# Optimization experiments

Hardware: AMD Instinct MI355X
Metric: run time of the kernel (lower is better)

## Reference

```python
import jax, jax.numpy as jnp
import numpy as np

B, S, D = 4, 4096, 1024  # S = maxlength * 2, D = hidden_dim * 2 (bi-rnn)
MAXLENGTH = 2048
NEG_BIG = -2.0 ** 31


def setup_inputs() -> dict:
    key = jax.random.key(0)
    k1, k2, k3, k4, k5 = jax.random.split(key, 5)
    inputs = jax.random.normal(k1, (B, S, D), dtype=jnp.float32)
    length = jax.random.randint(k2, (B,), 1, MAXLENGTH + 1, dtype=jnp.int32)
    # torch code requires max(length)*2 == maxlength*2 for expand() to work
    length = length.at[0].set(MAXLENGTH)
    scale = 1.0 / np.sqrt(D)
    Wq = jax.random.normal(k3, (D, D), dtype=jnp.float32) * scale
    Wk = jax.random.normal(k4, (D, D), dtype=jnp.float32) * scale
    Wv = jax.random.normal(k5, (D, D), dtype=jnp.float32) * scale
    return {"inputs": inputs, "length": length, "Wq": Wq, "Wk": Wk,
            "Wv": Wv, "maxlength": MAXLENGTH}


def reference(inputs, length, Wq, Wk, Wv, maxlength):
    # nn.Linear (bias=False): y = x @ W.T
    Q = inputs @ Wq.T                      # [B, S, D]
    K = inputs @ Wk.T                      # [B, S, D]
    V = inputs @ Wv.T                      # [B, S, D]
    max_len = maxlength * 2
    sent_len = length.astype(jnp.float32) * 2.0      # [B]
    # key-padding mask, broadcast over query dim: [B, 1, max_len]
    mask = (jnp.arange(max_len, dtype=jnp.float32)[None, :] < sent_len[:, None])[:, None, :]
    alpha = jnp.einsum('bqd,bkd->bqk', Q, K)         # [B, S, S] (no 1/sqrt(d) scaling, as in source)
    alpha = jnp.where(mask, alpha, NEG_BIG)
    alpha = jax.nn.softmax(alpha, axis=2)
    out = jnp.einsum('bqk,bkd->bqd', alpha, V)       # [B, S, D]
    return out
```

## Files before the change

### kernel.cpp

```cpp
#include <hip/hip_runtime.h>


typedef __attribute__((ext_vector_type(4))) float floatx4;
typedef __attribute__((ext_vector_type(4))) int intx4;
typedef __attribute__((ext_vector_type(8))) short shortx8;
typedef unsigned short ushort_t;

__device__ __forceinline__ ushort_t f2bf(float f) {
  union { float f; unsigned u; } x; x.f = f;
  unsigned r = x.u + 0x7fffu + ((x.u >> 16) & 1u);
  return (ushort_t)(r >> 16);
}
__device__ __forceinline__ float bf2f(ushort_t h) {
  union { unsigned u; float f; } x; x.u = ((unsigned)h) << 16; return x.f;
}
__device__ __forceinline__ void quant8(float v, char& qh, char& ql) {
  float vs = v * 16.0f;
  float h = rintf(vs);
  h = fminf(fmaxf(h, -127.f), 127.f);
  float l = rintf((vs - h) * 256.0f);
  l = fminf(fmaxf(l, -127.f), 127.f);
  qh = (char)(int)h; ql = (char)(int)l;
}
__device__ __forceinline__ void quant8w(float v, char& qh, char& ql) {
  float vs = v * 512.0f;
  float h = rintf(vs);
  h = fminf(fmaxf(h, -127.f), 127.f);
  float l = rintf((vs - h) * 256.0f);
  l = fminf(fmaxf(l, -127.f), 127.f);
  qh = (char)(int)h; ql = (char)(int)l;
}

__device__ __forceinline__ void gload_lds16(const void* g, void* l) {
  __builtin_amdgcn_global_load_lds(
      (__attribute__((address_space(1))) void*)(uintptr_t)g,
      (__attribute__((address_space(3))) void*)(unsigned)(uintptr_t)l,
      16, 0, 0);
}

template<int TM, int TN, int NA, int NB, int OMODE, int LMODE>
__global__ __launch_bounds__(256)
void gemm_bt(const ushort_t* __restrict__ A0g, const ushort_t* __restrict__ A1g,
             const ushort_t* __restrict__ B0g, const ushort_t* __restrict__ B1g,
             void* __restrict__ C0v, void* __restrict__ C1v,
             int K, int lda, int ldc, long bstride,
             const int* __restrict__ lenp, int b0, long sA, long sB, long sC)
{
  constexpr int BM = TM * 32, BN = TN * 32;
  constexpr int LA = TM / 2, LB = TN / 2;
  constexpr bool DUAL = (NA == 2) && (NB == 2);
  __shared__ ushort_t As[NA][BM][32];
  __shared__ ushort_t Bs[NB][BN][32];

  const int tid = threadIdx.x;
  const int z = blockIdx.z;
  const long row0 = (long)blockIdx.x * BM;
  const long col0 = (long)blockIdx.y * BN;

  int kend = K;
  if constexpr (LMODE == 2) {
    const int sent = lenp[b0 + z] * 2;
    kend = (sent + 127) & ~127;
  } else if constexpr (LMODE == 3) {
    const int sent = lenp[row0 >> 12] * 2;
    if ((int)(row0 & 4095) >= ((sent + 127) & ~127)) return;
  }

  const int sr = tid >> 2, scol = (tid & 3) * 8;
  const ushort_t* pA0 = A0g + z * sA + (row0 + sr) * (long)lda + scol;
  const ushort_t* pA1 = (NA == 2) ? A1g + z * sA + (row0 + sr) * (long)lda + scol : nullptr;
  const ushort_t* pB0 = B0g + z * sB + (col0 + sr) * (long)K + scol;
  const ushort_t* pB1 = (NB == 2) ? B1g + z * sB + (col0 + sr) * (long)K + scol : nullptr;
  ushort_t* lA0 = &As[0][sr][scol];
  ushort_t* lA1 = (NA == 2) ? &As[NA - 1][sr][scol] : nullptr;
  ushort_t* lB0 = &Bs[0][sr][scol];
  ushort_t* lB1 = (NB == 2) ? &Bs[NB - 1][sr][scol] : nullptr;
  const long jA = 64 * (long)lda, jB = 64 * (long)K;

  const int wid = tid >> 6, lane = tid & 63;
  const int wm = (wid >> 1) * (BM / 2), wn = (wid & 1) * (BN / 2);
  const int lr = lane & 15, lq = lane >> 4;

  floatx4 acc[TM][TN] = {};

  for (int k0 = 0; k0 < kend; k0 += 32) {
#pragma unroll
    for (int j = 0; j < LA; ++j) {
      gload_lds16(pA0 + k0 + j * jA, lA0 + j * 2048);
      if constexpr (NA == 2) gload_lds16(pA1 + k0 + j * jA, lA1 + j * 2048);
    }
#pragma unroll
    for (int j = 0; j < LB; ++j) {
      gload_lds16(pB0 + k0 + j * jB, lB0 + j * 2048);
      if constexpr (NB == 2) gload_lds16(pB1 + k0 + j * jB, lB1 + j * 2048);
    }
    __syncthreads();

    shortx8 ah[TM], al[TM], bh[TN], bl[TN];
#pragma unroll
    for (int t = 0; t < TM; ++t) {
      ah[t] = *(const shortx8*)&As[0][wm + t * 16 + lr][lq * 8];
      if constexpr (NA == 2) al[t] = *(const shortx8*)&As[1][wm + t * 16 + lr][lq * 8];
    }
#pragma unroll
    for (int t = 0; t < TN; ++t) {
      bh[t] = *(const shortx8*)&Bs[0][wn + t * 16 + lr][lq * 8];
      if constexpr (NB == 2) bl[t] = *(const shortx8*)&Bs[1][wn + t * 16 + lr][lq * 8];
    }
#pragma unroll
    for (int mt = 0; mt < TM; ++mt)
#pragma unroll
      for (int nt = 0; nt < TN; ++nt) {
        acc[mt][nt] = __builtin_amdgcn_mfma_f32_16x16x32_bf16(ah[mt], bh[nt], acc[mt][nt], 0, 0, 0);
        if constexpr (DUAL) {
          acc[mt][nt] = __builtin_amdgcn_mfma_f32_16x16x32_bf16(ah[mt], bl[nt], acc[mt][nt], 0, 0, 0);
          acc[mt][nt] = __builtin_amdgcn_mfma_f32_16x16x32_bf16(al[mt], bh[nt], acc[mt][nt], 0, 0, 0);
        }
      }
    __syncthreads();
  }

#pragma unroll
  for (int mt = 0; mt < TM; ++mt) {
#pragma unroll
    for (int nt = 0; nt < TN; ++nt) {
      long col = col0 + wn + nt * 16 + lr;
      if constexpr (OMODE == 2) {
        long row = row0 + wm + mt * 16 + lq * 4;
        long bb = row >> 12, s = row & 4095;
        ushort4 pk;
        pk.x = f2bf(acc[mt][nt][0]); pk.y = f2bf(acc[mt][nt][1]);
        pk.z = f2bf(acc[mt][nt][2]); pk.w = f2bf(acc[mt][nt][3]);
        *(ushort4*)&((ushort_t*)C0v)[bb * bstride + col * ldc + s] = pk;
      } else {
#pragma unroll
        for (int r = 0; r < 4; ++r) {
          long row = row0 + wm + mt * 16 + lq * 4 + r;
          float v = acc[mt][nt][r];
          if constexpr (OMODE == 0) {
            ((float*)C0v)[z * sC + row * ldc + col] = v;
          } else {
            char qh, ql;
            quant8(v, qh, ql);
            ((char*)C0v)[row * ldc + col] = qh;
            ((char*)C1v)[row * ldc + col] = ql;
          }
        }
      }
    }
  }
}

template<int LMODE>
__global__ __launch_bounds__(256)
void proj_i8(const char* __restrict__ Ah, const char* __restrict__ Al,
             const char* __restrict__ Bh, const char* __restrict__ Bl,
             char* __restrict__ Ch, char* __restrict__ Cl,
             const int* __restrict__ lenp)
{
  __shared__ char As[2][128][64];
  __shared__ char Bs[2][64][64];
  const int tid = threadIdx.x;
  const long row0 = (long)blockIdx.x * 128;
  const long col0 = (long)blockIdx.y * 64;
  if constexpr (LMODE == 3) {
    const int sent = lenp[row0 >> 12] * 2;
    if ((int)(row0 & 4095) >= ((sent + 127) & ~127)) return;
  }

  const int sr = tid >> 2, sc16 = (tid & 3) * 16;
  const char* pA0 = Ah + (row0 + sr) * 1024 + sc16;
  const char* pA1 = Al + (row0 + sr) * 1024 + sc16;
  const char* pB0 = Bh + (col0 + sr) * 1024 + sc16;
  const char* pB1 = Bl + (col0 + sr) * 1024 + sc16;
  char* lA0 = &As[0][sr][sc16];
  char* lA1 = &As[1][sr][sc16];
  char* lB0 = &Bs[0][sr][sc16];
  char* lB1 = &Bs[1][sr][sc16];

  const int wid = tid >> 6, lane = tid & 63;
  const int wm = (wid >> 1) * 64, wn = (wid & 1) * 32;
  const int lr = lane & 15, lq = lane >> 4;

  intx4 acc1[4][2] = {};
  intx4 acc2[4][2] = {};
  intx4 acc3[4][2] = {};

  for (int k0 = 0; k0 < 1024; k0 += 64) {
#pragma unroll
    for (int j = 0; j < 2; ++j) {
      gload_lds16(pA0 + k0 + j * 65536, lA0 + j * 4096);
      gload_lds16(pA1 + k0 + j * 65536, lA1 + j * 4096);
    }
    gload_lds16(pB0 + k0, lB0);
    gload_lds16(pB1 + k0, lB1);
    __syncthreads();

    intx4 ah[4], al[4], bh[2], bl[2];
#pragma unroll
    for (int t = 0; t < 4; ++t) {
      ah[t] = *(const intx4*)&As[0][wm + t * 16 + lr][lq * 16];
      al[t] = *(const intx4*)&As[1][wm + t * 16 + lr][lq * 16];
    }
#pragma unroll
    for (int t = 0; t < 2; ++t) {
      bh[t] = *(const intx4*)&Bs[0][wn + t * 16 + lr][lq * 16];
      bl[t] = *(const intx4*)&Bs[1][wn + t * 16 + lr][lq * 16];
    }
#pragma unroll
    for (int mt = 0; mt < 4; ++mt)
#pragma unroll
      for (int nt = 0; nt < 2; ++nt) {
        acc1[mt][nt] = __builtin_amdgcn_mfma_i32_16x16x64_i8(ah[mt], bh[nt], acc1[mt][nt], 0, 0, 0);
        acc2[mt][nt] = __builtin_amdgcn_mfma_i32_16x16x64_i8(ah[mt], bl[nt], acc2[mt][nt], 0, 0, 0);
        acc2[mt][nt] = __builtin_amdgcn_mfma_i32_16x16x64_i8(al[mt], bh[nt], acc2[mt][nt], 0, 0, 0);
        acc3[mt][nt] = __builtin_amdgcn_mfma_i32_16x16x64_i8(al[mt], bl[nt], acc3[mt][nt], 0, 0, 0);
      }
    __syncthreads();
  }

#pragma unroll
  for (int mt = 0; mt < 4; ++mt)
#pragma unroll
    for (int nt = 0; nt < 2; ++nt) {
      long col = col0 + wn + nt * 16 + lr;
#pragma unroll
      for (int r = 0; r < 4; ++r) {
        long row = row0 + wm + mt * 16 + lq * 4 + r;
        float v = ((float)acc1[mt][nt][r]
                   + (float)acc2[mt][nt][r] * (1.0f / 256.0f)
                   + (float)acc3[mt][nt][r] * (1.0f / 65536.0f)) * (1.0f / 8192.0f);
        char qh, ql;
        quant8(v, qh, ql);
        Ch[row * 1024 + col] = qh;
        Cl[row * 1024 + col] = ql;
      }
    }
}

__global__ __launch_bounds__(256)
void qk_i8(const char* __restrict__ Qh, const char* __restrict__ Ql,
           const char* __restrict__ Kh, const char* __restrict__ Kl,
           short* __restrict__ sc, const int* __restrict__ lenp, int b)
{
  __shared__ char As[2][128][64];
  __shared__ char Bs[2][64][64];
  const int tid = threadIdx.x;
  const long row0 = (long)blockIdx.x * 128;
  const long col0 = (long)blockIdx.y * 64;
  const int sent = lenp[b] * 2;
  if (col0 >= sent) return;

  const int sr = tid >> 2, sc16 = (tid & 3) * 16;
  const char* pA0 = Qh + (row0 + sr) * 1024 + sc16;
  const char* pA1 = Ql + (row0 + sr) * 1024 + sc16;
  const char* pB0 = Kh + (col0 + sr) * 1024 + sc16;
  const char* pB1 = Kl + (col0 + sr) * 1024 + sc16;
  char* lA0 = &As[0][sr][sc16];
  char* lA1 = &As[1][sr][sc16];
  char* lB0 = &Bs[0][sr][sc16];
  char* lB1 = &Bs[1][sr][sc16];

  const int wid = tid >> 6, lane = tid & 63;
  const int wm = (wid >> 1) * 64, wn = (wid & 1) * 32;
  const int lr = lane & 15, lq = lane >> 4;

  intx4 acc1[4][2] = {};
  intx4 acc2[4][2] = {};

  for (int k0 = 0; k0 < 1024; k0 += 64) {
#pragma unroll
    for (int j = 0; j < 2; ++j) {
      gload_lds16(pA0 + k0 + j * 65536, lA0 + j * 4096);
      gload_lds16(pA1 + k0 + j * 65536, lA1 + j * 4096);
    }
    gload_lds16(pB0 + k0, lB0);
    gload_lds16(pB1 + k0, lB1);
    __syncthreads();

    intx4 ah[4], al[4], bh[2], bl[2];
#pragma unroll
    for (int t = 0; t < 4; ++t) {
      ah[t] = *(const intx4*)&As[0][wm + t * 16 + lr][lq * 16];
      al[t] = *(const intx4*)&As[1][wm + t * 16 + lr][lq * 16];
    }
#pragma unroll
    for (int t = 0; t < 2; ++t) {
      bh[t] = *(const intx4*)&Bs[0][wn + t * 16 + lr][lq * 16];
      bl[t] = *(const intx4*)&Bs[1][wn + t * 16 + lr][lq * 16];
    }
#pragma unroll
    for (int mt = 0; mt < 4; ++mt)
#pragma unroll
      for (int nt = 0; nt < 2; ++nt) {
        acc1[mt][nt] = __builtin_amdgcn_mfma_i32_16x16x64_i8(ah[mt], bh[nt], acc1[mt][nt], 0, 0, 0);
        acc2[mt][nt] = __builtin_amdgcn_mfma_i32_16x16x64_i8(ah[mt], bl[nt], acc2[mt][nt], 0, 0, 0);
        acc2[mt][nt] = __builtin_amdgcn_mfma_i32_16x16x64_i8(al[mt], bh[nt], acc2[mt][nt], 0, 0, 0);
      }
    __syncthreads();
  }

#pragma unroll
  for (int mt = 0; mt < 4; ++mt)
#pragma unroll
    for (int nt = 0; nt < 2; ++nt) {
      long col = col0 + wn + nt * 16 + lr;
#pragma unroll
      for (int r = 0; r < 4; ++r) {
        long row = row0 + wm + mt * 16 + lq * 4 + r;
        float v = (float)acc1[mt][nt][r] * 0.125f
                + (float)acc2[mt][nt][r] * (1.0f / 2048.0f);
        v = fminf(fmaxf(v, -32000.0f), 32000.0f);
        sc[row * 4096 + col] = (short)(int)rintf(v);
      }
    }
}

__global__ __launch_bounds__(256)
void cast_split(const float* __restrict__ in, ushort_t* __restrict__ hi,
                char* __restrict__ qh, char* __restrict__ ql, int n4) {
  int i = blockIdx.x * 256 + threadIdx.x;
  if (i < n4) {
    float4 v = ((const float4*)in)[i];
    ushort4 h;
    h.x = f2bf(v.x); h.y = f2bf(v.y); h.z = f2bf(v.z); h.w = f2bf(v.w);
    ((ushort4*)hi)[i] = h;
    char ax, bx, ay, by, az, bz, aw, bw;
    quant8(v.x, ax, bx); quant8(v.y, ay, by);
    quant8(v.z, az, bz); quant8(v.w, aw, bw);
    char4 a, b;
    a.x = ax; a.y = ay; a.z = az; a.w = aw;
    b.x = bx; b.y = by; b.z = bz; b.w = bw;
    ((char4*)qh)[i] = a;
    ((char4*)ql)[i] = b;
  }
}

__global__ __launch_bounds__(256)
void cast_wqk(const float* __restrict__ w0, const float* __restrict__ w1,
              char* __restrict__ h0, char* __restrict__ l0,
              char* __restrict__ h1, char* __restrict__ l1, int n4) {
  int i = blockIdx.x * 256 + threadIdx.x;
  if (i >= n4) return;
  const float* in = blockIdx.y ? w1 : w0;
  char* hp = blockIdx.y ? h1 : h0;
  char* lp = blockIdx.y ? l1 : l0;
  float4 v = ((const float4*)in)[i];
  char ax, bx, ay, by, az, bz, aw, bw;
  quant8w(v.x, ax, bx); quant8w(v.y, ay, by);
  quant8w(v.z, az, bz); quant8w(v.w, aw, bw);
  char4 a, b;
  a.x = ax; a.y = ay; a.z = az; a.w = aw;
  b.x = bx; b.y = by; b.z = bz; b.w = bw;
  ((char4*)hp)[i] = a;
  ((char4*)lp)[i] = b;
}

__global__ __launch_bounds__(256)
void cast_wv(const float* __restrict__ w, ushort_t* __restrict__ h, int n4) {
  int i = blockIdx.x * 256 + threadIdx.x;
  if (i >= n4) return;
  float4 v = ((const float4*)w)[i];
  ushort4 p;
  p.x = f2bf(v.x); p.y = f2bf(v.y); p.z = f2bf(v.z); p.w = f2bf(v.w);
  ((ushort4*)h)[i] = p;
}

__global__ __launch_bounds__(256)
void softmax_rows(short* __restrict__ scores, const int* __restrict__ length, int b0) {
  const long row = blockIdx.x;
  const int b = b0 + (int)(row >> 12);
  short* p = scores + row * 4096;
  const int sent = length[b] * 2;
  const int sentceil = (sent + 127) & ~127;
  const int tid = threadIdx.x;
  float vals[16];
  float mx = -3.4e38f;
  int nj = 0;
  for (int c = tid; c < sentceil; c += 256) {
    float v = (float)p[c] * (1.0f / 32.0f);
    v = (c < sent) ? v : -2147483648.0f;
    vals[nj++] = v;
    mx = fmaxf(mx, v);
  }
#pragma unroll
  for (int off = 32; off > 0; off >>= 1) mx = fmaxf(mx, __shfl_down(mx, off));
  __shared__ float red[8];
  if ((tid & 63) == 0) red[tid >> 6] = mx;
  __syncthreads();
  mx = fmaxf(fmaxf(red[0], red[1]), fmaxf(red[2], red[3]));
  float sum = 0.f;
  for (int j = 0; j < nj; ++j) { vals[j] = __expf(vals[j] - mx); sum += vals[j]; }
#pragma unroll
  for (int off = 32; off > 0; off >>= 1) sum += __shfl_down(sum, off);
  __syncthreads();
  if ((tid & 63) == 0) red[tid >> 6] = sum;
  __syncthreads();
  float inv = 1.0f / (red[0] + red[1] + red[2] + red[3]);
  ushort_t* pb = (ushort_t*)p;
  int j = 0;
  for (int c = tid; c < sentceil; c += 256) pb[c] = f2bf(vals[j++] * inv);
}

extern "C" void kernel_launch(void* const* d_in, const int* in_sizes, int n_in,
                              void* d_out, int out_size, void* d_ws, size_t ws_size,
                              hipStream_t stream) {
  const float* X   = (const float*)d_in[0];
  const int*   len = (const int*)d_in[1];
  const float* Wq  = (const float*)d_in[2];
  const float* Wk  = (const float*)d_in[3];
  const float* Wv  = (const float*)d_in[4];
  float* out = (float*)d_out;

  const int Bn = 4, S = 4096, D = 1024;
  const long MS = (long)Bn * S;

  char* w = (char*)d_ws;
  ushort_t* Xhi = (ushort_t*)w; w += MS * D * 2;
  char* Xh8 = w; w += MS * D;
  char* Xl8 = w; w += MS * D;
  char* Qh8 = w; w += MS * D;
  char* Ql8 = w; w += MS * D;
  char* Kh8 = w; w += MS * D;
  char* Kl8 = w; w += MS * D;
  ushort_t* Vt  = (ushort_t*)w; w += MS * D * 2;
  char* Wqh8 = w; w += (long)D * D;
  char* Wql8 = w; w += (long)D * D;
  char* Wkh8 = w; w += (long)D * D;
  char* Wkl8 = w; w += (long)D * D;
  ushort_t* Wvh = (ushort_t*)w; w += (long)D * D * 2;
  short* sc = (short*)d_ws;

  const int n4x = (int)(MS * D / 4);
  const int n4w = D * D / 4;
  cast_split<<<(n4x + 255) / 256, 256, 0, stream>>>(X, Xhi, Xh8, Xl8, n4x);
  cast_wqk<<<dim3((n4w + 255) / 256, 2), 256, 0, stream>>>(
      Wq, Wk, Wqh8, Wql8, Wkh8, Wkl8, n4w);
  cast_wv<<<(n4w + 255) / 256, 256, 0, stream>>>(Wv, Wvh, n4w);

  dim3 blk(256);
  proj_i8<0><<<dim3(MS / 128, D / 64), blk, 0, stream>>>(
      Xh8, Xl8, Wqh8, Wql8, Qh8, Ql8, len);
  proj_i8<3><<<dim3(MS / 128, D / 64), blk, 0, stream>>>(
      Xh8, Xl8, Wkh8, Wkl8, Kh8, Kl8, len);
  gemm_bt<4, 4, 1, 1, 2, 3><<<dim3(MS / 128, D / 128, 1), blk, 0, stream>>>(
      Xhi, nullptr, Wvh, nullptr, Vt, nullptr, D, D, S, (long)D * S,
      len, 0, 0, 0, 0);

  for (int b = 0; b < Bn; ++b) {
    const long so = (long)b * S * D;
    qk_i8<<<dim3(S / 128, S / 64), blk, 0, stream>>>(
        Qh8 + so, Ql8 + so, Kh8 + so, Kl8 + so, sc, len, b);
    softmax_rows<<<S, 256, 0, stream>>>(sc, len, b);
    gemm_bt<4, 2, 1, 1, 0, 2><<<dim3(S / 128, D / 64, 1), blk, 0, stream>>>(
        (const ushort_t*)sc, nullptr, Vt + (long)b * D * S, nullptr,
        out + so, nullptr, S, S, D, 0, len, b, 0, 0, 0);
  }
}
```

Before: 717.7 us.

## Double-buffer LDS tiles with vmcnt-based prefetch in all GEMM kernels

Adds double-buffered shared-memory staging to gemm_bt, proj_i8 and qk_i8. The next K tile is issued with global_load_lds before computing on the current one, and the code waits with explicit s_waitcnt vmcnt counts plus raw barriers, so load latency overlaps MFMA work. It also strips the unused dual/quant modes from gemm_bt and widens the PV GEMM tile from 128x64 to 128x128. The doubled LDS footprint may lower occupancy, and the hand-counted vmcnt waits are fragile if the compiler reorders memory operations.

```diff
diff --git a/kernel.cpp b/kernel.cpp
--- a/kernel.cpp
+++ b/kernel.cpp
@@ -38,28 +38,38 @@
       16, 0, 0);
 }
 
-template<int TM, int TN, int NA, int NB, int OMODE, int LMODE>
-__global__ __launch_bounds__(256)
-void gemm_bt(const ushort_t* __restrict__ A0g, const ushort_t* __restrict__ A1g,
-             const ushort_t* __restrict__ B0g, const ushort_t* __restrict__ B1g,
-             void* __restrict__ C0v, void* __restrict__ C1v,
-             int K, int lda, int ldc, long bstride,
-             const int* __restrict__ lenp, int b0, long sA, long sB, long sC)
+template<int N> __device__ __forceinline__ void wait_vm() {
+  static_assert(N == 0 || N == 4 || N == 6, "unsupported vmcnt");
+  if constexpr (N == 0) asm volatile("s_waitcnt vmcnt(0)" ::: "memory");
+  else if constexpr (N == 4) asm volatile("s_waitcnt vmcnt(4)" ::: "memory");
+  else if constexpr (N == 6) asm volatile("s_waitcnt vmcnt(6)" ::: "memory");
+}
+__device__ __forceinline__ void barrier_fenced() {
+  asm volatile("" ::: "memory");
+  __builtin_amdgcn_s_barrier();
+  asm volatile("" ::: "memory");
+}
+
+template<int TM, int TN, int OMODE, int LMODE>
+__global__ __launch_bounds__(256)
+void gemm_bt(const ushort_t* __restrict__ A0g, const ushort_t* __restrict__ B0g,
+             void* __restrict__ C0v, int K, int lda, int ldc, long bstride,
+             const int* __restrict__ lenp, int b0)
 {
   constexpr int BM = TM * 32, BN = TN * 32;
   constexpr int LA = TM / 2, LB = TN / 2;
-  constexpr bool DUAL = (NA == 2) && (NB == 2);
-  __shared__ ushort_t As[NA][BM][32];
-  __shared__ ushort_t Bs[NB][BN][32];
+  constexpr int NL = LA + LB;
+  constexpr int BUFA = BM * 32, BUFB = BN * 32;
+  __shared__ ushort_t As[2][BM][32];
+  __shared__ ushort_t Bs[2][BN][32];
 
   const int tid = threadIdx.x;
-  const int z = blockIdx.z;
   const long row0 = (long)blockIdx.x * BM;
   const long col0 = (long)blockIdx.y * BN;
 
   int kend = K;
   if constexpr (LMODE == 2) {
-    const int sent = lenp[b0 + z] * 2;
+    const int sent = lenp[b0] * 2;
     kend = (sent + 127) & ~127;
   } else if constexpr (LMODE == 3) {
     const int sent = lenp[row0 >> 12] * 2;
@@ -67,14 +77,10 @@
   }
 
   const int sr = tid >> 2, scol = (tid & 3) * 8;
-  const ushort_t* pA0 = A0g + z * sA + (row0 + sr) * (long)lda + scol;
-  const ushort_t* pA1 = (NA == 2) ? A1g + z * sA + (row0 + sr) * (long)lda + scol : nullptr;
-  const ushort_t* pB0 = B0g + z * sB + (col0 + sr) * (long)K + scol;
-  const ushort_t* pB1 = (NB == 2) ? B1g + z * sB + (col0 + sr) * (long)K + scol : nullptr;
-  ushort_t* lA0 = &As[0][sr][scol];
-  ushort_t* lA1 = (NA == 2) ? &As[NA - 1][sr][scol] : nullptr;
-  ushort_t* lB0 = &Bs[0][sr][scol];
-  ushort_t* lB1 = (NB == 2) ? &Bs[NB - 1][sr][scol] : nullptr;
+  const ushort_t* pA = A0g + (row0 + sr) * (long)lda + scol;
+  const ushort_t* pB = B0g + (col0 + sr) * (long)K + scol;
+  ushort_t* lA = &As[0][sr][scol];
+  ushort_t* lB = &Bs[0][sr][scol];
   const long jA = 64 * (long)lda, jB = 64 * (long)K;
 
   const int wid = tid >> 6, lane = tid & 63;
@@ -83,41 +89,37 @@
 
   floatx4 acc[TM][TN] = {};
 
-  for (int k0 = 0; k0 < kend; k0 += 32) {
-#pragma unroll
-    for (int j = 0; j < LA; ++j) {
-      gload_lds16(pA0 + k0 + j * jA, lA0 + j * 2048);
-      if constexpr (NA == 2) gload_lds16(pA1 + k0 + j * jA, lA1 + j * 2048);
-    }
-#pragma unroll
-    for (int j = 0; j < LB; ++j) {
-      gload_lds16(pB0 + k0 + j * jB, lB0 + j * 2048);
-      if constexpr (NB == 2) gload_lds16(pB1 + k0 + j * jB, lB1 + j * 2048);
-    }
-    __syncthreads();
-
-    shortx8 ah[TM], al[TM], bh[TN], bl[TN];
-#pragma unroll
-    for (int t = 0; t < TM; ++t) {
-      ah[t] = *(const shortx8*)&As[0][wm + t * 16 + lr][lq * 8];
-      if constexpr (NA == 2) al[t] = *(const shortx8*)&As[1][wm + t * 16 + lr][lq * 8];
-    }
-#pragma unroll
-    for (int t = 0; t < TN; ++t) {
-      bh[t] = *(const shortx8*)&Bs[0][wn + t * 16 + lr][lq * 8];
-      if constexpr (NB == 2) bl[t] = *(const shortx8*)&Bs[1][wn + t * 16 + lr][lq * 8];
-    }
+  auto stage = [&](int buf, int k0) {
+#pragma unroll
+    for (int j = 0; j < LA; ++j)
+      gload_lds16(pA + k0 + j * jA, lA + buf * BUFA + j * 2048);
+#pragma unroll
+    for (int j = 0; j < LB; ++j)
+      gload_lds16(pB + k0 + j * jB, lB + buf * BUFB + j * 2048);
+  };
+
+  const int nk = kend >> 5;
+  stage(0, 0);
+  for (int t = 0; t < nk; ++t) {
+    const int cur = t & 1;
+    if (t + 1 < nk) { stage(cur ^ 1, (t + 1) << 5); wait_vm<NL>(); }
+    else           { wait_vm<0>(); }
+    barrier_fenced();
+
+    shortx8 af[TM], bf[TN];
+#pragma unroll
+    for (int tt = 0; tt < TM; ++tt)
+      af[tt] = *(const shortx8*)&As[cur][wm + tt * 16 + lr][lq * 8];
+#pragma unroll
+    for (int tt = 0; tt < TN; ++tt)
+      bf[tt] = *(const shortx8*)&Bs[cur][wn + tt * 16 + lr][lq * 8];
 #pragma unroll
     for (int mt = 0; mt < TM; ++mt)
 #pragma unroll
-      for (int nt = 0; nt < TN; ++nt) {
-        acc[mt][nt] = __builtin_amdgcn_mfma_f32_16x16x32_bf16(ah[mt], bh[nt], acc[mt][nt], 0, 0, 0);
-        if constexpr (DUAL) {
-          acc[mt][nt] = __builtin_amdgcn_mfma_f32_16x16x32_bf16(ah[mt], bl[nt], acc[mt][nt], 0, 0, 0);
-          acc[mt][nt] = __builtin_amdgcn_mfma_f32_16x16x32_bf16(al[mt], bh[nt], acc[mt][nt], 0, 0, 0);
-        }
-      }
-    __syncthreads();
+      for (int nt = 0; nt < TN; ++nt)
+        acc[mt][nt] = __builtin_amdgcn_mfma_f32_16x16x32_bf16(af[mt], bf[nt], acc[mt][nt], 0, 0, 0);
+
+    barrier_fenced();
   }
 
 #pragma unroll
@@ -136,15 +138,7 @@
 #pragma unroll
         for (int r = 0; r < 4; ++r) {
           long row = row0 + wm + mt * 16 + lq * 4 + r;
-          float v = acc[mt][nt][r];
-          if constexpr (OMODE == 0) {
-            ((float*)C0v)[z * sC + row * ldc + col] = v;
-          } else {
-            char qh, ql;
-            quant8(v, qh, ql);
-            ((char*)C0v)[row * ldc + col] = qh;
-            ((char*)C1v)[row * ldc + col] = ql;
-          }
+          ((float*)C0v)[row * ldc + col] = acc[mt][nt][r];
         }
       }
     }
@@ -158,8 +152,8 @@
              char* __restrict__ Ch, char* __restrict__ Cl,
              const int* __restrict__ lenp)
 {
-  __shared__ char As[2][128][64];
-  __shared__ char Bs[2][64][64];
+  __shared__ char As[2][2][128][64];
+  __shared__ char Bs[2][2][64][64];
   const int tid = threadIdx.x;
   const long row0 = (long)blockIdx.x * 128;
   const long col0 = (long)blockIdx.y * 64;
@@ -173,10 +167,10 @@
   const char* pA1 = Al + (row0 + sr) * 1024 + sc16;
   const char* pB0 = Bh + (col0 + sr) * 1024 + sc16;
   const char* pB1 = Bl + (col0 + sr) * 1024 + sc16;
-  char* lA0 = &As[0][sr][sc16];
-  char* lA1 = &As[1][sr][sc16];
-  char* lB0 = &Bs[0][sr][sc16];
-  char* lB1 = &Bs[1][sr][sc16];
+  char* lA0 = &As[0][0][sr][sc16];
+  char* lA1 = &As[0][1][sr][sc16];
+  char* lB0 = &Bs[0][0][sr][sc16];
+  char* lB1 = &Bs[0][1][sr][sc16];
 
   const int wid = tid >> 6, lane = tid & 63;
   const int wm = (wid >> 1) * 64, wn = (wid & 1) * 32;
@@ -186,26 +180,33 @@
   intx4 acc2[4][2] = {};
   intx4 acc3[4][2] = {};
 
-  for (int k0 = 0; k0 < 1024; k0 += 64) {
+  auto stage = [&](int buf, int k0) {
 #pragma unroll
     for (int j = 0; j < 2; ++j) {
-      gload_lds16(pA0 + k0 + j * 65536, lA0 + j * 4096);
-      gload_lds16(pA1 + k0 + j * 65536, lA1 + j * 4096);
-    }
-    gload_lds16(pB0 + k0, lB0);
-    gload_lds16(pB1 + k0, lB1);
-    __syncthreads();
+      gload_lds16(pA0 + k0 + j * 65536, lA0 + buf * 16384 + j * 4096);
+      gload_lds16(pA1 + k0 + j * 65536, lA1 + buf * 16384 + j * 4096);
+    }
+    gload_lds16(pB0 + k0, lB0 + buf * 8192);
+    gload_lds16(pB1 + k0, lB1 + buf * 8192);
+  };
+
+  stage(0, 0);
+  for (int t = 0; t < 16; ++t) {
+    const int cur = t & 1;
+    if (t + 1 < 16) { stage(cur ^ 1, (t + 1) << 6); wait_vm<6>(); }
+    else           { wait_vm<0>(); }
+    barrier_fenced();
 
     intx4 ah[4], al[4], bh[2], bl[2];
 #pragma unroll
-    for (int t = 0; t < 4; ++t) {
-      ah[t] = *(const intx4*)&As[0][wm + t * 16 + lr][lq * 16];
-      al[t] = *(const intx4*)&As[1][wm + t * 16 + lr][lq * 16];
-    }
-#pragma unroll
-    for (int t = 0; t < 2; ++t) {
-      bh[t] = *(const intx4*)&Bs[0][wn + t * 16 + lr][lq * 16];
-      bl[t] = *(const intx4*)&Bs[1][wn + t * 16 + lr][lq * 16];
+    for (int tt = 0; tt < 4; ++tt) {
+      ah[tt] = *(const intx4*)&As[cur][0][wm + tt * 16 + lr][lq * 16];
+      al[tt] = *(const intx4*)&As[cur][1][wm + tt * 16 + lr][lq * 16];
+    }
+#pragma unroll
+    for (int tt = 0; tt < 2; ++tt) {
+      bh[tt] = *(const intx4*)&Bs[cur][0][wn + tt * 16 + lr][lq * 16];
+      bl[tt] = *(const intx4*)&Bs[cur][1][wn + tt * 16 + lr][lq * 16];
     }
 #pragma unroll
     for (int mt = 0; mt < 4; ++mt)
@@ -216,7 +217,7 @@
         acc2[mt][nt] = __builtin_amdgcn_mfma_i32_16x16x64_i8(al[mt], bh[nt], acc2[mt][nt], 0, 0, 0);
         acc3[mt][nt] = __builtin_amdgcn_mfma_i32_16x16x64_i8(al[mt], bl[nt], acc3[mt][nt], 0, 0, 0);
       }
-    __syncthreads();
+    barrier_fenced();
   }
 
 #pragma unroll
@@ -243,8 +244,8 @@
            const char* __restrict__ Kh, const char* __restrict__ Kl,
            short* __restrict__ sc, const int* __restrict__ lenp, int b)
 {
-  __shared__ char As[2][128][64];
-  __shared__ char Bs[2][64][64];
+  __shared__ char As[2][2][128][64];
+  __shared__ char Bs[2][2][64][64];
   const int tid = threadIdx.x;
   const long row0 = (long)blockIdx.x * 128;
   const long col0 = (long)blockIdx.y * 64;
@@ -256,10 +257,10 @@
   const char* pA1 = Ql + (row0 + sr) * 1024 + sc16;
   const char* pB0 = Kh + (col0 + sr) * 1024 + sc16;
   const char* pB1 = Kl + (col0 + sr) * 1024 + sc16;
-  char* lA0 = &As[0][sr][sc16];
-  char* lA1 = &As[1][sr][sc16];
-  char* lB0 = &Bs[0][sr][sc16];
-  char* lB1 = &Bs[1][sr][sc16];
+  char* lA0 = &As[0][0][sr][sc16];
+  char* lA1 = &As[0][1][sr][sc16];
+  char* lB0 = &Bs[0][0][sr][sc16];
+  char* lB1 = &Bs[0][1][sr][sc16];
 
   const int wid = tid >> 6, lane = tid & 63;
   const int wm = (wid >> 1) * 64, wn = (wid & 1) * 32;
@@ -268,26 +269,33 @@
   intx4 acc1[4][2] = {};
   intx4 acc2[4][2] = {};
 
-  for (int k0 = 0; k0 < 1024; k0 += 64) {
+  auto stage = [&](int buf, int k0) {
 #pragma unroll
     for (int j = 0; j < 2; ++j) {
-      gload_lds16(pA0 + k0 + j * 65536, lA0 + j * 4096);
-      gload_lds16(pA1 + k0 + j * 65536, lA1 + j * 4096);
-    }
-    gload_lds16(pB0 + k0, lB0);
-    gload_lds16(pB1 + k0, lB1);
-    __syncthreads();
+      gload_lds16(pA0 + k0 + j * 65536, lA0 + buf * 16384 + j * 4096);
+      gload_lds16(pA1 + k0 + j * 65536, lA1 + buf * 16384 + j * 4096);
+    }
+    gload_lds16(pB0 + k0, lB0 + buf * 8192);
+    gload_lds16(pB1 + k0, lB1 + buf * 8192);
+  };
+
+  stage(0, 0);
+  for (int t = 0; t < 16; ++t) {
+    const int cur = t & 1;
+    if (t + 1 < 16) { stage(cur ^ 1, (t + 1) << 6); wait_vm<6>(); }
+    else           { wait_vm<0>(); }
+    barrier_fenced();
 
     intx4 ah[4], al[4], bh[2], bl[2];
 #pragma unroll
-    for (int t = 0; t < 4; ++t) {
-      ah[t] = *(const intx4*)&As[0][wm + t * 16 + lr][lq * 16];
-      al[t] = *(const intx4*)&As[1][wm + t * 16 + lr][lq * 16];
-    }
-#pragma unroll
-    for (int t = 0; t < 2; ++t) {
-      bh[t] = *(const intx4*)&Bs[0][wn + t * 16 + lr][lq * 16];
-      bl[t] = *(const intx4*)&Bs[1][wn + t * 16 + lr][lq * 16];
+    for (int tt = 0; tt < 4; ++tt) {
+      ah[tt] = *(const intx4*)&As[cur][0][wm + tt * 16 + lr][lq * 16];
+      al[tt] = *(const intx4*)&As[cur][1][wm + tt * 16 + lr][lq * 16];
+    }
+#pragma unroll
+    for (int tt = 0; tt < 2; ++tt) {
+      bh[tt] = *(const intx4*)&Bs[cur][0][wn + tt * 16 + lr][lq * 16];
+      bl[tt] = *(const intx4*)&Bs[cur][1][wn + tt * 16 + lr][lq * 16];
     }
 #pragma unroll
     for (int mt = 0; mt < 4; ++mt)
@@ -297,7 +305,7 @@
         acc2[mt][nt] = __builtin_amdgcn_mfma_i32_16x16x64_i8(ah[mt], bl[nt], acc2[mt][nt], 0, 0, 0);
         acc2[mt][nt] = __builtin_amdgcn_mfma_i32_16x16x64_i8(al[mt], bh[nt], acc2[mt][nt], 0, 0, 0);
       }
-    __syncthreads();
+    barrier_fenced();
   }
 
 #pragma unroll
@@ -443,17 +451,15 @@
       Xh8, Xl8, Wqh8, Wql8, Qh8, Ql8, len);
   proj_i8<3><<<dim3(MS / 128, D / 64), blk, 0, stream>>>(
       Xh8, Xl8, Wkh8, Wkl8, Kh8, Kl8, len);
-  gemm_bt<4, 4, 1, 1, 2, 3><<<dim3(MS / 128, D / 128, 1), blk, 0, stream>>>(
-      Xhi, nullptr, Wvh, nullptr, Vt, nullptr, D, D, S, (long)D * S,
-      len, 0, 0, 0, 0);
+  gemm_bt<4, 4, 2, 3><<<dim3(MS / 128, D / 128), blk, 0, stream>>>(
+      Xhi, Wvh, Vt, D, D, S, (long)D * S, len, 0);
 
   for (int b = 0; b < Bn; ++b) {
     const long so = (long)b * S * D;
     qk_i8<<<dim3(S / 128, S / 64), blk, 0, stream>>>(
         Qh8 + so, Ql8 + so, Kh8 + so, Kl8 + so, sc, len, b);
     softmax_rows<<<S, 256, 0, stream>>>(sc, len, b);
-    gemm_bt<4, 2, 1, 1, 0, 2><<<dim3(S / 128, D / 64, 1), blk, 0, stream>>>(
-        (const ushort_t*)sc, nullptr, Vt + (long)b * D * S, nullptr,
-        out + so, nullptr, S, S, D, 0, len, b, 0, 0, 0);
-  }
-}
+    gemm_bt<4, 4, 0, 2><<<dim3(S / 128, D / 128), blk, 0, stream>>>(
+        (const ushort_t*)sc, Vt + (long)b * D * S, out + so, S, S, D, 0, len, b);
+  }
+}
```

After: 652.2 us. 1.1x faster.
